# Optimization experiments

Measured on AMD Instinct MI355X. Metric: run time of the kernel, lower is better.

Reference implementation:

```python
import jax, jax.numpy as jnp
import numpy as np

N = 100000
E = 600000
H = 128
G = 64          # number of graphs
LN_EPS = 1e-5


def setup_inputs() -> dict:
    key = jax.random.key(0)
    ks = jax.random.split(key, 16)
    node = jax.random.normal(ks[0], (N, H), dtype=jnp.float32)
    edge_index = jax.random.randint(ks[1], (2, E), 0, N, dtype=jnp.int64)
    edge_attr = jax.random.normal(ks[2], (E, 1), dtype=jnp.float32)
    batch_ptr = jnp.sort(jax.random.randint(ks[3], (N,), 0, G, dtype=jnp.int64))
    s = 1.0 / np.sqrt(H)
    params = dict(
        eps=jnp.float32(0.0),  # GINConv train_eps=True, init 0
        W1=jax.random.uniform(ks[4], (H, H), jnp.float32, -s, s),
        b1=jnp.zeros((H,), jnp.float32),
        g1=jnp.ones((H,), jnp.float32), be1=jnp.zeros((H,), jnp.float32),
        W2=jax.random.uniform(ks[5], (H, H), jnp.float32, -s, s),
        b2=jnp.zeros((H,), jnp.float32),
        g2=jnp.ones((H,), jnp.float32), be2=jnp.zeros((H,), jnp.float32),
        W3=jax.random.uniform(ks[6], (H, H), jnp.float32, -s, s),
        b3=jnp.zeros((H,), jnp.float32),
        ln_w=jnp.ones((H,), jnp.float32), ln_b=jnp.zeros((H,), jnp.float32),
    )
    return dict(node=node, edge_index=edge_index, edge_attr=edge_attr,
                batch_ptr=batch_ptr, **params)


def _layernorm(x, g, b):
    mu = x.mean(-1, keepdims=True)
    var = ((x - mu) ** 2).mean(-1, keepdims=True)
    return (x - mu) * jax.lax.rsqrt(var + LN_EPS) * g + b


def _forward(node, edge_index, batch_ptr, eps, W1, b1, g1, be1, W2, b2, g2, be2,
             W3, b3, ln_w, ln_b):
    src, dst = edge_index[0], edge_index[1]
    # GIN sum aggregation: scatter-add neighbor features to targets
    agg = jax.ops.segment_sum(node[src], dst, num_segments=N)  # [N, H]
    h = (1.0 + eps) * node + agg
    # 3-layer MLP (PyG MLP: lin -> LayerNorm -> ReLU, final lin plain)
    h = jax.nn.relu(_layernorm(h @ W1 + b1, g1, be1))
    h = jax.nn.relu(_layernorm(h @ W2 + b2, g2, be2))
    h = h @ W3 + b3
    # PyG graph-mode LayerNorm: normalize over all nodes+features per graph
    cnt = jax.ops.segment_sum(jnp.ones((N,), h.dtype), batch_ptr, num_segments=G)
    norm = jnp.maximum(cnt * H, 1.0)                       # [G]
    mean = jax.ops.segment_sum(h.sum(-1), batch_ptr, num_segments=G) / norm
    hc = h - mean[batch_ptr][:, None]
    var = jax.ops.segment_sum((hc * hc).sum(-1), batch_ptr, num_segments=G) / norm
    out = hc * jax.lax.rsqrt(var + LN_EPS)[batch_ptr][:, None] * ln_w + ln_b
    return jax.nn.relu(out)


def reference(node, edge_index, edge_attr, batch_ptr, eps, W1, b1, g1, be1,
              W2, b2, g2, be2, W3, b3, ln_w, ln_b):
    del edge_attr  # accepted by GIN_Layer.forward but unused
    return _forward(node, edge_index, batch_ptr, eps, W1, b1, g1, be1,
                    W2, b2, g2, be2, W3, b3, ln_w, ln_b)
```

## Files before the change

kernel.cpp:

```cpp
#include <hip/hip_runtime.h>

#define N_NODES 100000
#define N_EDGES 600000
#define H 128
#define G_NUM 64
#define LN_EPS 1e-5f

#define WSTR 136

#define NTILES ((N_NODES + 63) / 64)

#define SCAN_CHUNK 1024
#define SCAN_NB ((N_NODES + SCAN_CHUNK - 1) / SCAN_CHUNK)
#define FILL_NB ((N_EDGES + 255) / 256)
#define WT_NB ((3 * 16384 + 255) / 256)

#define SCRATCH_PW 1088

typedef __attribute__((ext_vector_type(8))) short short8;
typedef __attribute__((ext_vector_type(4))) float floatx4;

__device__ __forceinline__ unsigned short f2bf(float x) {
    unsigned int u = __float_as_uint(x);
    u += 0x7fffu + ((u >> 16) & 1u);
    return (unsigned short)(u >> 16);
}
__device__ __forceinline__ float bf2f(unsigned short h) {
    return __uint_as_float(((unsigned int)h) << 16);
}

__global__ __launch_bounds__(256) void hist_kernel(
    const int* __restrict__ ei, int* __restrict__ deg)
{
    int e = blockIdx.x * 256 + threadIdx.x;
    if (e >= N_EDGES) return;
    atomicAdd(&deg[ei[N_EDGES + e]], 1);
}

__global__ __launch_bounds__(256) void scan1_kernel(
    const int* __restrict__ deg, int* __restrict__ off,
    int* __restrict__ blksum)
{
    __shared__ int sA[256], sB[256];
    const int tid = threadIdx.x;
    const int base = blockIdx.x * SCAN_CHUNK + tid * 4;
    int v[4];
#pragma unroll
    for (int j = 0; j < 4; ++j) {
        int i = base + j;
        v[j] = (i < N_NODES) ? deg[i] : 0;
    }
    int tsum = v[0] + v[1] + v[2] + v[3];
    int* a = sA; int* b = sB;
    a[tid] = tsum;
    __syncthreads();
#pragma unroll
    for (int o = 1; o < 256; o <<= 1) {
        int t = a[tid] + ((tid >= o) ? a[tid - o] : 0);
        b[tid] = t;
        __syncthreads();
        int* tmp = a; a = b; b = tmp;
    }
    int run = a[tid] - tsum;
#pragma unroll
    for (int j = 0; j < 4; ++j) {
        int i = base + j;
        if (i < N_NODES) off[i] = run;
        run += v[j];
    }
    if (tid == 255) blksum[blockIdx.x] = a[255];
}

__global__ __launch_bounds__(256) void scan23_kernel(
    int* __restrict__ off, const int* __restrict__ blksum,
    int* __restrict__ cursor)
{
    __shared__ int sA[128], sB[128];
    const int tid = threadIdx.x;
    if (tid < 128) sA[tid] = (tid < SCAN_NB) ? blksum[tid] : 0;
    __syncthreads();
    int* a = sA; int* b = sB;
#pragma unroll
    for (int o = 1; o < 128; o <<= 1) {
        int t = 0;
        if (tid < 128) t = a[tid] + ((tid >= o) ? a[tid - o] : 0);
        __syncthreads();
        if (tid < 128) b[tid] = t;
        __syncthreads();
        int* tmp = a; a = b; b = tmp;
    }
    int excl = 0;
    if (tid < 128) excl = a[tid] - ((tid < SCAN_NB) ? blksum[tid] : 0);
    __syncthreads();
    if (tid < 128) sA[tid] = excl;
    __syncthreads();

    int i = blockIdx.x * 256 + tid;
    if (i < N_NODES) {
        int val = off[i] + sA[i >> 10];
        off[i] = val;
        cursor[i] = val;
    }
    if (i == 0) off[N_NODES] = N_EDGES;
}

__global__ __launch_bounds__(256) void fill_wt_kernel(
    const int* __restrict__ ei, int* __restrict__ cursor,
    int* __restrict__ csr,
    const float* __restrict__ W1, const float* __restrict__ W2,
    const float* __restrict__ W3, unsigned short* __restrict__ WT)
{
    int gb = blockIdx.x;
    if (gb < FILL_NB) {
        int e = gb * 256 + threadIdx.x;
        if (e >= N_EDGES) return;
        int dst = ei[N_EDGES + e];
        int pos = atomicAdd(&cursor[dst], 1);
        csr[pos] = ei[e];
    } else {
        int idx = (gb - FILL_NB) * 256 + threadIdx.x;
        if (idx >= 3 * 16384) return;
        int l = idx >> 14, r = idx & 16383;
        int k = r >> 7, n = r & 127;
        const float* W = (l == 0) ? W1 : ((l == 1) ? W2 : W3);
        WT[l * 16384 + n * 128 + k] = f2bf(W[k * 128 + n]);
    }
}

__device__ __forceinline__ void stageWb(unsigned short* __restrict__ Wb,
                                        const unsigned short* __restrict__ WT,
                                        int tid)
{
#pragma unroll
    for (int t = 0; t < 8; ++t) {
        int c = tid + t * 256;
        int row = c >> 4, c8 = c & 15;
        *(short8*)&Wb[row * WSTR + c8 * 8] = *(const short8*)&WT[row * 128 + c8 * 8];
    }
}

__device__ __forceinline__ void gemm_frags(const unsigned short* __restrict__ hIn,
                                           const unsigned short* __restrict__ Wb,
                                           floatx4 acc[8], int w, int lane)
{
    const int c = lane & 15, q = lane >> 4;
#pragma unroll
    for (int nt = 0; nt < 8; ++nt) acc[nt] = (floatx4){0.f, 0.f, 0.f, 0.f};
#pragma unroll
    for (int kt = 0; kt < 4; ++kt) {
        short8 a = *(const short8*)&hIn[(w * 16 + c) * WSTR + kt * 32 + q * 8];
#pragma unroll
        for (int nt = 0; nt < 8; ++nt) {
            short8 b = *(const short8*)&Wb[(nt * 16 + c) * WSTR + kt * 32 + q * 8];
            acc[nt] = __builtin_amdgcn_mfma_f32_16x16x32_bf16(a, b, acc[nt], 0, 0, 0);
        }
    }
}

__device__ __forceinline__ void gemm_layer(const unsigned short* __restrict__ hIn,
                                           unsigned short* __restrict__ hOut,
                                           const unsigned short* __restrict__ Wb,
                                           const float* __restrict__ bias,
                                           int w, int lane)
{
    const int c = lane & 15, q = lane >> 4;
    floatx4 acc[8];
    gemm_frags(hIn, Wb, acc, w, lane);
#pragma unroll
    for (int nt = 0; nt < 8; ++nt) {
        float bv = bias[nt * 16 + c];
#pragma unroll
        for (int i = 0; i < 4; ++i)
            hOut[(w * 16 + q * 4 + i) * WSTR + nt * 16 + c] = f2bf(acc[nt][i] + bv);
    }
}

__device__ __forceinline__ void ln_pass(unsigned short* __restrict__ buf,
                                        const float* __restrict__ g,
                                        const float* __restrict__ be, int tid)
{
    const int row = tid >> 2, qt = tid & 3;
    unsigned short* rb = buf + row * WSTR + qt * 32;
    float v[32];
    float sum = 0.f, sq = 0.f;
#pragma unroll
    for (int j = 0; j < 4; ++j) {
        short8 t = *(const short8*)&rb[j * 8];
#pragma unroll
        for (int e = 0; e < 8; ++e) {
            float f = bf2f((unsigned short)t[e]);
            v[j * 8 + e] = f; sum += f; sq += f * f;
        }
    }
    sum += __shfl_xor(sum, 1); sum += __shfl_xor(sum, 2);
    sq  += __shfl_xor(sq, 1);  sq  += __shfl_xor(sq, 2);
    const float mu   = sum * (1.0f / 128.0f);
    const float rstd = rsqrtf(sq * (1.0f / 128.0f) - mu * mu + LN_EPS);
#pragma unroll
    for (int j = 0; j < 4; ++j) {
        const float4 g0 = *(const float4*)&g[qt * 32 + j * 8];
        const float4 g1 = *(const float4*)&g[qt * 32 + j * 8 + 4];
        const float4 e0 = *(const float4*)&be[qt * 32 + j * 8];
        const float4 e1 = *(const float4*)&be[qt * 32 + j * 8 + 4];
        const float gw[8] = {g0.x, g0.y, g0.z, g0.w, g1.x, g1.y, g1.z, g1.w};
        const float bw[8] = {e0.x, e0.y, e0.z, e0.w, e1.x, e1.y, e1.z, e1.w};
        short8 o;
#pragma unroll
        for (int e = 0; e < 8; ++e) {
            float val = fmaxf(0.f, (v[j * 8 + e] - mu) * rstd * gw[e] + bw[e]);
            o[e] = (short)f2bf(val);
        }
        *(short8*)&rb[j * 8] = o;
    }
}

__global__ __launch_bounds__(256) void fused_mlp_kernel(
    const float* __restrict__ node, const int* __restrict__ off,
    const int* __restrict__ csr, const float* __restrict__ epsp,
    const unsigned short* __restrict__ WT,
    const float* __restrict__ b1, const float* __restrict__ g1,
    const float* __restrict__ be1,
    const float* __restrict__ b2, const float* __restrict__ g2,
    const float* __restrict__ be2,
    const float* __restrict__ b3, const int* __restrict__ batch,
    float* __restrict__ out, float* __restrict__ gstat)
{
    __shared__ unsigned short Wb[128 * WSTR];
    __shared__ unsigned short hA[64 * WSTR];
    __shared__ unsigned short hB[64 * WSTR];
    __shared__ float prm[7 * 128];
    __shared__ float s_gsum[G_NUM], s_gsq[G_NUM], s_gcnt[G_NUM];

    const int tid = threadIdx.x;
    const int w = tid >> 6, lane = tid & 63;
    const int row0 = blockIdx.x * 64;

    if (tid < G_NUM) { s_gsum[tid] = 0.f; s_gsq[tid] = 0.f; s_gcnt[tid] = 0.f; }
    {
        const float* srcs[7] = {b1, g1, be1, b2, g2, be2, b3};
#pragma unroll
        for (int t = 0; t < 4; ++t) {
            int i = tid + t * 256;
            if (i < 7 * 128) prm[i] = srcs[i >> 7][i & 127];
        }
    }
    stageWb(Wb, WT, tid);

    {
        const float2* np2 = (const float2*)node;
        const float epsv = 1.0f + epsp[0];
        const int n0 = row0 + w * 16;
        int oidx = n0 + ((lane < 17) ? lane : 16);
        if (oidx > N_NODES) oidx = N_NODES;
        const int offl = off[oidx];
        const int e_begin = __shfl(offl, 0);
        const int e_end   = __shfl(offl, 16);
        const int cnt = e_end - e_begin;

        float2 acc[16];
#pragma unroll
        for (int i = 0; i < 16; ++i) {
            int n = n0 + i;
            if (n < N_NODES) {
                float2 own = np2[(size_t)n * 64 + lane];
                acc[i].x = epsv * own.x; acc[i].y = epsv * own.y;
            } else {
                acc[i].x = 0.f; acc[i].y = 0.f;
            }
        }

        if (cnt <= SCRATCH_PW) {
            int* scr = ((int*)hB) + w * SCRATCH_PW;
            for (int k = lane; k < cnt; k += 64) scr[k] = csr[e_begin + k];
            __threadfence_block();

#pragma unroll
            for (int g4 = 0; g4 < 4; ++g4) {
                int p[4], e[4];
#pragma unroll
                for (int j = 0; j < 4; ++j) {
                    p[j] = __shfl(offl, g4 * 4 + j) - e_begin;
                    e[j] = __shfl(offl, g4 * 4 + j + 1) - e_begin;
                }
                float2 vc[4]; bool ac[4];
#pragma unroll
                for (int j = 0; j < 4; ++j) {
                    ac[j] = p[j] < e[j];
                    vc[j] = make_float2(0.f, 0.f);
                    if (ac[j]) {
                        int s = scr[p[j]];
                        vc[j] = np2[(size_t)s * 64 + lane];
                    }
                }
                while (ac[0] || ac[1] || ac[2] || ac[3]) {
                    float2 vn[4]; bool an[4];
#pragma unroll
                    for (int j = 0; j < 4; ++j) {
                        an[j] = (p[j] + 1) < e[j];
                        vn[j] = make_float2(0.f, 0.f);
                        if (an[j]) {
                            int s = scr[p[j] + 1];
                            vn[j] = np2[(size_t)s * 64 + lane];
                        }
                    }
#pragma unroll
                    for (int j = 0; j < 4; ++j) {
                        if (ac[j]) {
                            acc[g4 * 4 + j].x += vc[j].x;
                            acc[g4 * 4 + j].y += vc[j].y;
                            p[j] += 1;
                        }
                        ac[j] = an[j];
                        vc[j] = vn[j];
                    }
                }
            }
        } else {
            for (int i = 0; i < 16; ++i) {
                int n = n0 + i;
                if (n >= N_NODES) continue;
                for (int j = off[n]; j < off[n + 1]; ++j) {
                    float2 v = np2[(size_t)csr[j] * 64 + lane];
                    acc[i].x += v.x; acc[i].y += v.y;
                }
            }
        }
#pragma unroll
        for (int i = 0; i < 16; ++i) {
            unsigned int pack = (unsigned)f2bf(acc[i].x) |
                                ((unsigned)f2bf(acc[i].y) << 16);
            ((unsigned int*)&hA[(w * 16 + i) * WSTR])[lane] = pack;
        }
    }
    __syncthreads();

    gemm_layer(hA, hB, Wb, &prm[0], w, lane);
    ln_pass(hB, &prm[128], &prm[256], tid);
    __syncthreads();
    stageWb(Wb, WT + 16384, tid);
    __syncthreads();

    gemm_layer(hB, hA, Wb, &prm[384], w, lane);
    ln_pass(hA, &prm[512], &prm[640], tid);
    __syncthreads();
    stageWb(Wb, WT + 32768, tid);
    __syncthreads();

    {
        const int c = lane & 15, q = lane >> 4;
        floatx4 acc3[8];
        gemm_frags(hA, Wb, acc3, w, lane);
        float sum[4] = {0.f, 0.f, 0.f, 0.f};
        float sq[4]  = {0.f, 0.f, 0.f, 0.f};
#pragma unroll
        for (int nt = 0; nt < 8; ++nt) {
            float bv = prm[768 + nt * 16 + c];
#pragma unroll
            for (int i = 0; i < 4; ++i) {
                float vv = acc3[nt][i] + bv;
                size_t nrow = (size_t)row0 + w * 16 + q * 4 + i;
                if (nrow < N_NODES)
                    out[nrow * H + nt * 16 + c] = vv;
                sum[i] += vv; sq[i] += vv * vv;
            }
        }
#pragma unroll
        for (int m = 1; m < 16; m <<= 1) {
#pragma unroll
            for (int i = 0; i < 4; ++i) {
                sum[i] += __shfl_xor(sum[i], m);
                sq[i]  += __shfl_xor(sq[i], m);
            }
        }
        if (c == 0) {
#pragma unroll
            for (int i = 0; i < 4; ++i) {
                size_t nrow = (size_t)row0 + w * 16 + q * 4 + i;
                if (nrow < N_NODES) {
                    int g = batch[nrow];
                    atomicAdd(&s_gsum[g], sum[i]);
                    atomicAdd(&s_gsq[g], sq[i]);
                    atomicAdd(&s_gcnt[g], 1.0f);
                }
            }
        }
    }
    __syncthreads();
    if (tid < G_NUM && s_gcnt[tid] > 0.f) {
        unsafeAtomicAdd(&gstat[tid], s_gsum[tid]);
        unsafeAtomicAdd(&gstat[G_NUM + tid], s_gsq[tid]);
        unsafeAtomicAdd(&gstat[2 * G_NUM + tid], s_gcnt[tid]);
    }
}

__global__ void finalize_stats_kernel(float* __restrict__ gstat)
{
    int g = threadIdx.x;
    if (g < G_NUM) {
        float cnt  = gstat[2 * G_NUM + g];
        float norm = fmaxf(cnt * (float)H, 1.0f);
        float mean = gstat[g] / norm;
        float var  = gstat[G_NUM + g] / norm - mean * mean;
        gstat[3 * G_NUM + g] = mean;
        gstat[4 * G_NUM + g] = rsqrtf(var + LN_EPS);
    }
}

__global__ __launch_bounds__(256) void final_ln_kernel(
    float* __restrict__ h3, const int* __restrict__ batch,
    const float* __restrict__ lnw, const float* __restrict__ lnb,
    const float* __restrict__ gstat)
{
    int idx4 = blockIdx.x * 256 + threadIdx.x;
    if (idx4 >= N_NODES * 32) return;
    int node = idx4 >> 5;
    int c4 = (idx4 & 31) * 4;
    int g = batch[node];
    float mean = gstat[3 * G_NUM + g];
    float inv  = gstat[4 * G_NUM + g];
    float4 v = ((const float4*)h3)[idx4];
    float4 w = *(const float4*)&lnw[c4];
    float4 b = *(const float4*)&lnb[c4];
    v.x = fmaxf(0.f, (v.x - mean) * inv * w.x + b.x);
    v.y = fmaxf(0.f, (v.y - mean) * inv * w.y + b.y);
    v.z = fmaxf(0.f, (v.z - mean) * inv * w.z + b.z);
    v.w = fmaxf(0.f, (v.w - mean) * inv * w.w + b.w);
    ((float4*)h3)[idx4] = v;
}

extern "C" void kernel_launch(void* const* d_in, const int* in_sizes, int n_in,
                              void* d_out, int out_size, void* d_ws, size_t ws_size,
                              hipStream_t stream)
{
    const float* node  = (const float*)d_in[0];
    const int*   ei    = (const int*)d_in[1];
    const int*   batch = (const int*)d_in[3];
    const float* epsp  = (const float*)d_in[4];
    const float* W1    = (const float*)d_in[5];
    const float* b1    = (const float*)d_in[6];
    const float* g1    = (const float*)d_in[7];
    const float* be1   = (const float*)d_in[8];
    const float* W2    = (const float*)d_in[9];
    const float* b2    = (const float*)d_in[10];
    const float* g2    = (const float*)d_in[11];
    const float* be2   = (const float*)d_in[12];
    const float* W3    = (const float*)d_in[13];
    const float* b3    = (const float*)d_in[14];
    const float* lnw   = (const float*)d_in[15];
    const float* lnb   = (const float*)d_in[16];

    float* out = (float*)d_out;

    float* gstat  = (float*)d_ws;
    int*   deg    = (int*)d_ws + 512;
    int*   off    = deg + N_NODES;
    int*   cursor = off + N_NODES + 1;
    int*   csr    = cursor + N_NODES;
    int*   blksum = csr + N_EDGES;
    unsigned short* WT = (unsigned short*)((int*)d_ws + 900612);

    hipMemsetAsync(d_ws, 0, (512 + N_NODES) * sizeof(int), stream);

    hist_kernel<<<(N_EDGES + 255) / 256, 256, 0, stream>>>(ei, deg);
    scan1_kernel<<<SCAN_NB, 256, 0, stream>>>(deg, off, blksum);
    scan23_kernel<<<(N_NODES + 255) / 256, 256, 0, stream>>>(off, blksum, cursor);
    fill_wt_kernel<<<FILL_NB + WT_NB, 256, 0, stream>>>(ei, cursor, csr,
                                                        W1, W2, W3, WT);

    fused_mlp_kernel<<<NTILES, 256, 0, stream>>>(
        node, off, csr, epsp, WT, b1, g1, be1, b2, g2, be2, b3, batch,
        out, gstat);

    finalize_stats_kernel<<<1, 64, 0, stream>>>(gstat);

    final_ln_kernel<<<(N_NODES * 32 + 255) / 256, 256, 0, stream>>>(
        out, batch, lnw, lnb, gstat);
}
```

Before: 353.8 us.

## Fuse LayerNorm into GEMM epilogue, read weights from global, drop finalize kernel

```diff
diff --git a/kernel.cpp b/kernel.cpp
--- a/kernel.cpp
+++ b/kernel.cpp
@@ -24,9 +24,6 @@
     unsigned int u = __float_as_uint(x);
     u += 0x7fffu + ((u >> 16) & 1u);
     return (unsigned short)(u >> 16);
-}
-__device__ __forceinline__ float bf2f(unsigned short h) {
-    return __uint_as_float(((unsigned int)h) << 16);
 }
 
 __global__ __launch_bounds__(256) void hist_kernel(
@@ -127,20 +124,8 @@
     }
 }
 
-__device__ __forceinline__ void stageWb(unsigned short* __restrict__ Wb,
-                                        const unsigned short* __restrict__ WT,
-                                        int tid)
-{
-#pragma unroll
-    for (int t = 0; t < 8; ++t) {
-        int c = tid + t * 256;
-        int row = c >> 4, c8 = c & 15;
-        *(short8*)&Wb[row * WSTR + c8 * 8] = *(const short8*)&WT[row * 128 + c8 * 8];
-    }
-}
-
 __device__ __forceinline__ void gemm_frags(const unsigned short* __restrict__ hIn,
-                                           const unsigned short* __restrict__ Wb,
+                                           const unsigned short* __restrict__ WTl,
                                            floatx4 acc[8], int w, int lane)
 {
     const int c = lane & 15, q = lane >> 4;
@@ -151,70 +136,63 @@
         short8 a = *(const short8*)&hIn[(w * 16 + c) * WSTR + kt * 32 + q * 8];
 #pragma unroll
         for (int nt = 0; nt < 8; ++nt) {
-            short8 b = *(const short8*)&Wb[(nt * 16 + c) * WSTR + kt * 32 + q * 8];
+            short8 b = *(const short8*)&WTl[(nt * 16 + c) * 128 + kt * 32 + q * 8];
             acc[nt] = __builtin_amdgcn_mfma_f32_16x16x32_bf16(a, b, acc[nt], 0, 0, 0);
         }
     }
 }
 
-__device__ __forceinline__ void gemm_layer(const unsigned short* __restrict__ hIn,
-                                           unsigned short* __restrict__ hOut,
-                                           const unsigned short* __restrict__ Wb,
-                                           const float* __restrict__ bias,
-                                           int w, int lane)
+__device__ __forceinline__ void gemm_layer_ln(const unsigned short* __restrict__ hIn,
+                                              unsigned short* __restrict__ hOut,
+                                              const unsigned short* __restrict__ WTl,
+                                              const float* __restrict__ bias,
+                                              const float* __restrict__ g,
+                                              const float* __restrict__ be,
+                                              int w, int lane)
 {
     const int c = lane & 15, q = lane >> 4;
     floatx4 acc[8];
-    gemm_frags(hIn, Wb, acc, w, lane);
+    gemm_frags(hIn, WTl, acc, w, lane);
+
+    float sum[4] = {0.f, 0.f, 0.f, 0.f};
+    float sq[4]  = {0.f, 0.f, 0.f, 0.f};
 #pragma unroll
     for (int nt = 0; nt < 8; ++nt) {
         float bv = bias[nt * 16 + c];
 #pragma unroll
-        for (int i = 0; i < 4; ++i)
-            hOut[(w * 16 + q * 4 + i) * WSTR + nt * 16 + c] = f2bf(acc[nt][i] + bv);
-    }
-}
-
-__device__ __forceinline__ void ln_pass(unsigned short* __restrict__ buf,
-                                        const float* __restrict__ g,
-                                        const float* __restrict__ be, int tid)
-{
-    const int row = tid >> 2, qt = tid & 3;
-    unsigned short* rb = buf + row * WSTR + qt * 32;
-    float v[32];
-    float sum = 0.f, sq = 0.f;
-#pragma unroll
-    for (int j = 0; j < 4; ++j) {
-        short8 t = *(const short8*)&rb[j * 8];
-#pragma unroll
-        for (int e = 0; e < 8; ++e) {
-            float f = bf2f((unsigned short)t[e]);
-            v[j * 8 + e] = f; sum += f; sq += f * f;
-        }
-    }
-    sum += __shfl_xor(sum, 1); sum += __shfl_xor(sum, 2);
-    sq  += __shfl_xor(sq, 1);  sq  += __shfl_xor(sq, 2);
-    const float mu   = sum * (1.0f / 128.0f);
-    const float rstd = rsqrtf(sq * (1.0f / 128.0f) - mu * mu + LN_EPS);
-#pragma unroll
-    for (int j = 0; j < 4; ++j) {
-        const float4 g0 = *(const float4*)&g[qt * 32 + j * 8];
-        const float4 g1 = *(const float4*)&g[qt * 32 + j * 8 + 4];
-        const float4 e0 = *(const float4*)&be[qt * 32 + j * 8];
-        const float4 e1 = *(const float4*)&be[qt * 32 + j * 8 + 4];
-        const float gw[8] = {g0.x, g0.y, g0.z, g0.w, g1.x, g1.y, g1.z, g1.w};
-        const float bw[8] = {e0.x, e0.y, e0.z, e0.w, e1.x, e1.y, e1.z, e1.w};
-        short8 o;
-#pragma unroll
-        for (int e = 0; e < 8; ++e) {
-            float val = fmaxf(0.f, (v[j * 8 + e] - mu) * rstd * gw[e] + bw[e]);
-            o[e] = (short)f2bf(val);
-        }
-        *(short8*)&rb[j * 8] = o;
-    }
-}
-
-__global__ __launch_bounds__(256) void fused_mlp_kernel(
+        for (int i = 0; i < 4; ++i) {
+            float vv = acc[nt][i] + bv;
+            acc[nt][i] = vv;
+            sum[i] += vv; sq[i] += vv * vv;
+        }
+    }
+#pragma unroll
+    for (int m = 1; m < 16; m <<= 1) {
+#pragma unroll
+        for (int i = 0; i < 4; ++i) {
+            sum[i] += __shfl_xor(sum[i], m);
+            sq[i]  += __shfl_xor(sq[i], m);
+        }
+    }
+    float mu[4], rstd[4];
+#pragma unroll
+    for (int i = 0; i < 4; ++i) {
+        mu[i]   = sum[i] * (1.0f / 128.0f);
+        rstd[i] = rsqrtf(sq[i] * (1.0f / 128.0f) - mu[i] * mu[i] + LN_EPS);
+    }
+#pragma unroll
+    for (int nt = 0; nt < 8; ++nt) {
+        float gw = g[nt * 16 + c];
+        float bw = be[nt * 16 + c];
+#pragma unroll
+        for (int i = 0; i < 4; ++i) {
+            float val = fmaxf(0.f, (acc[nt][i] - mu[i]) * rstd[i] * gw + bw);
+            hOut[(w * 16 + q * 4 + i) * WSTR + nt * 16 + c] = f2bf(val);
+        }
+    }
+}
+
+__global__ __launch_bounds__(256, 4) void fused_mlp_kernel(
     const float* __restrict__ node, const int* __restrict__ off,
     const int* __restrict__ csr, const float* __restrict__ epsp,
     const unsigned short* __restrict__ WT,
@@ -225,7 +203,6 @@
     const float* __restrict__ b3, const int* __restrict__ batch,
     float* __restrict__ out, float* __restrict__ gstat)
 {
-    __shared__ unsigned short Wb[128 * WSTR];
     __shared__ unsigned short hA[64 * WSTR];
     __shared__ unsigned short hB[64 * WSTR];
     __shared__ float prm[7 * 128];
@@ -244,7 +221,6 @@
             if (i < 7 * 128) prm[i] = srcs[i >> 7][i & 127];
         }
     }
-    stageWb(Wb, WT, tid);
 
     {
         const float2* np2 = (const float2*)node;
@@ -334,22 +310,13 @@
     }
     __syncthreads();
 
-    gemm_layer(hA, hB, Wb, &prm[0], w, lane);
-    ln_pass(hB, &prm[128], &prm[256], tid);
-    __syncthreads();
-    stageWb(Wb, WT + 16384, tid);
-    __syncthreads();
-
-    gemm_layer(hB, hA, Wb, &prm[384], w, lane);
-    ln_pass(hA, &prm[512], &prm[640], tid);
-    __syncthreads();
-    stageWb(Wb, WT + 32768, tid);
-    __syncthreads();
+    gemm_layer_ln(hA, hB, WT,         &prm[0],   &prm[128], &prm[256], w, lane);
+    gemm_layer_ln(hB, hA, WT + 16384, &prm[384], &prm[512], &prm[640], w, lane);
 
     {
         const int c = lane & 15, q = lane >> 4;
         floatx4 acc3[8];
-        gemm_frags(hA, Wb, acc3, w, lane);
+        gemm_frags(hA, WT + 32768, acc3, w, lane);
         float sum[4] = {0.f, 0.f, 0.f, 0.f};
         float sq[4]  = {0.f, 0.f, 0.f, 0.f};
 #pragma unroll
@@ -393,19 +360,6 @@
     }
 }
 
-__global__ void finalize_stats_kernel(float* __restrict__ gstat)
-{
-    int g = threadIdx.x;
-    if (g < G_NUM) {
-        float cnt  = gstat[2 * G_NUM + g];
-        float norm = fmaxf(cnt * (float)H, 1.0f);
-        float mean = gstat[g] / norm;
-        float var  = gstat[G_NUM + g] / norm - mean * mean;
-        gstat[3 * G_NUM + g] = mean;
-        gstat[4 * G_NUM + g] = rsqrtf(var + LN_EPS);
-    }
-}
-
 __global__ __launch_bounds__(256) void final_ln_kernel(
     float* __restrict__ h3, const int* __restrict__ batch,
     const float* __restrict__ lnw, const float* __restrict__ lnb,
@@ -416,8 +370,13 @@
     int node = idx4 >> 5;
     int c4 = (idx4 & 31) * 4;
     int g = batch[node];
-    float mean = gstat[3 * G_NUM + g];
-    float inv  = gstat[4 * G_NUM + g];
+    float s   = gstat[g];
+    float qq  = gstat[G_NUM + g];
+    float cnt = gstat[2 * G_NUM + g];
+    float norm = fmaxf(cnt * (float)H, 1.0f);
+    float mean = s / norm;
+    float var  = qq / norm - mean * mean;
+    float inv  = rsqrtf(var + LN_EPS);
     float4 v = ((const float4*)h3)[idx4];
     float4 w = *(const float4*)&lnw[c4];
     float4 b = *(const float4*)&lnb[c4];
@@ -471,8 +430,6 @@
         node, off, csr, epsp, WT, b1, g1, be1, b2, g2, be2, b3, batch,
         out, gstat);
 
-    finalize_stats_kernel<<<1, 64, 0, stream>>>(gstat);
-
     final_ln_kernel<<<(N_NODES * 32 + 255) / 256, 256, 0, stream>>>(
         out, batch, lnw, lnb, gstat);
 }
```

Result: faster. 345.9 us (-2.2%).
